# Optimization experiments

Hardware: AMD Instinct MI355X
Metric: run time of the kernel (lower is better)

## Reference

```python
import jax, jax.numpy as jnp
import numpy as np

N_NODES = 100000
N_EDGES = 1600000
F_IN = 256
HID = 256
N_CLS = 16
NUM_PROP = 3


def setup_inputs() -> dict:
    key = jax.random.key(0)
    ks = jax.random.split(key, 8)
    x = jax.random.normal(ks[0], (N_NODES, F_IN), dtype=jnp.float32)
    edge_index = jax.random.randint(ks[1], (2, N_EDGES), 0, N_NODES, dtype=jnp.int64)
    # Glorot-ish scaled weights
    W1 = jax.random.normal(ks[2], (F_IN, HID), dtype=jnp.float32) / np.sqrt(F_IN)
    b1 = jnp.zeros((HID,), dtype=jnp.float32)
    Wi = jax.random.normal(ks[3], (HID, HID), dtype=jnp.float32) / np.sqrt(HID)
    bi = jnp.zeros((HID,), dtype=jnp.float32)
    W2 = jax.random.normal(ks[4], (HID, N_CLS), dtype=jnp.float32) / np.sqrt(HID)
    b2 = jnp.zeros((N_CLS,), dtype=jnp.float32)
    return {"x": x, "edge_index": edge_index, "W1": W1, "b1": b1,
            "Wi": Wi, "bi": bi, "W2": W2, "b2": b2}


def _gcn_graph(edge_index, n_nodes, dtype):
    # PyG GCNConv default: add self-loops, symmetric normalization.
    loop = jnp.arange(n_nodes, dtype=edge_index.dtype)
    src = jnp.concatenate([edge_index[0], loop])  # message source (x_j)
    dst = jnp.concatenate([edge_index[1], loop])  # aggregation target
    deg = jax.ops.segment_sum(jnp.ones_like(dst, dtype=dtype), dst, num_segments=n_nodes)
    dis = jnp.where(deg > 0, jax.lax.rsqrt(jnp.maximum(deg, 1.0)), 0.0)
    norm = dis[src] * dis[dst]  # [E+N]
    return src, dst, norm


def _gcn_conv(h, W, b, src, dst, norm, n_nodes):
    h = h @ W                                   # [N, out]
    msg = h[src] * norm[:, None]                # gather + scale, [E+N, out]
    out = jax.ops.segment_sum(msg, dst, num_segments=n_nodes)
    return out + b


def reference(x, edge_index, W1, b1, Wi, bi, W2, b2):
    n = x.shape[0]
    src, dst, norm = _gcn_graph(edge_index, n, x.dtype)
    h = _gcn_conv(x, W1, b1, src, dst, norm, n)
    # dropout p=0.25 is identity in eval mode (training=False)
    for _ in range(NUM_PROP):
        h = _gcn_conv(h, Wi, bi, src, dst, norm, n)
    h = jax.nn.relu(h)
    h = _gcn_conv(h, W2, b2, src, dst, norm, n)
    return jax.nn.softmax(h, axis=0)  # Softmax(dim=0): over nodes
```

## Files before the change

### kernel.cpp

```cpp
#include <hip/hip_runtime.h>
#include <cstdint>
#include <cstddef>

#define NFEAT 256
#define NCLS  16

typedef unsigned int uint;
typedef unsigned short ushort;
typedef __attribute__((ext_vector_type(8))) short short8;
typedef __attribute__((ext_vector_type(4))) float f32x4;

__device__ inline float blo(uint u) { return __uint_as_float(u << 16); }
__device__ inline float bhi(uint u) { return __uint_as_float(u & 0xffff0000u); }
__device__ inline ushort f2bf(float f) {
    uint b = __float_as_uint(f);
    b += 0x7fffu + ((b >> 16) & 1u);
    return (ushort)(b >> 16);
}
__device__ inline uint pack2(float a, float b) {
    return (uint)f2bf(a) | ((uint)f2bf(b) << 16);
}


__global__ __launch_bounds__(256) void k_ccount(const int* __restrict__ dst,
                                                int* __restrict__ bhist, int E, int nb) {
    __shared__ int h[512];
    int t = threadIdx.x;
    for (int i = t; i < nb; i += 256) h[i] = 0;
    __syncthreads();
    for (int i = blockIdx.x * 256 + t; i < E; i += gridDim.x * 256)
        atomicAdd(&h[dst[i] >> 8], 1);
    __syncthreads();
    for (int i = t; i < nb; i += 256)
        if (h[i]) atomicAdd(&bhist[i], h[i]);
}

__global__ __launch_bounds__(256) void k_cscan(const int* __restrict__ bhist,
                                               int* __restrict__ boff,
                                               int* __restrict__ gcur,
                                               int* __restrict__ rowptr,
                                               int nb, int Nn) {
    int t = threadIdx.x;
    int v0 = (2 * t < nb) ? bhist[2 * t] : 0;
    int v1 = (2 * t + 1 < nb) ? bhist[2 * t + 1] : 0;
    int s = v0 + v1;
    __shared__ int ps[256];
    ps[t] = s;
    __syncthreads();
    for (int off = 1; off < 256; off <<= 1) {
        int v = (t >= off) ? ps[t - off] : 0;
        __syncthreads();
        ps[t] += v;
        __syncthreads();
    }
    int ex = ps[t] - s;
    if (2 * t < nb)     { boff[2 * t] = ex;          gcur[2 * t] = ex; }
    if (2 * t + 1 < nb) { boff[2 * t + 1] = ex + v0; gcur[2 * t + 1] = ex + v0; }
    if (t == 255) { boff[nb] = ps[255]; rowptr[Nn] = ps[255]; }
}

__global__ __launch_bounds__(256) void k_cfill(const int* __restrict__ src,
                                               const int* __restrict__ dst,
                                               int* __restrict__ gcur,
                                               uint2* __restrict__ ebuf, int E, int nb) {
    __shared__ int hist[400];
    __shared__ int lstart[400];
    __shared__ int gbase[400];
    __shared__ int cur[400];
    __shared__ int ps[256];
    __shared__ uint2 stg[4096];
    __shared__ ushort sb[4096];
    int t = threadIdx.x;
    int base = blockIdx.x * 4096;
    int lim = min(4096, E - base);
    for (int i = t; i < nb; i += 256) hist[i] = 0;
    __syncthreads();
    for (int k = t; k < lim; k += 256) atomicAdd(&hist[dst[base + k] >> 8], 1);
    __syncthreads();
    int v0 = (2 * t < nb) ? hist[2 * t] : 0;
    int v1 = (2 * t + 1 < nb) ? hist[2 * t + 1] : 0;
    int s = v0 + v1;
    ps[t] = s;
    __syncthreads();
    for (int off = 1; off < 256; off <<= 1) {
        int v = (t >= off) ? ps[t - off] : 0;
        __syncthreads();
        ps[t] += v;
        __syncthreads();
    }
    int ex = ps[t] - s;
    if (2 * t < nb) {
        lstart[2 * t] = ex; cur[2 * t] = ex;
        if (v0) gbase[2 * t] = atomicAdd(&gcur[2 * t], v0);
    }
    if (2 * t + 1 < nb) {
        lstart[2 * t + 1] = ex + v0; cur[2 * t + 1] = ex + v0;
        if (v1) gbase[2 * t + 1] = atomicAdd(&gcur[2 * t + 1], v1);
    }
    __syncthreads();
    for (int k = t; k < lim; k += 256) {
        int s_ = src[base + k], d_ = dst[base + k];
        int b = d_ >> 8;
        int slot = atomicAdd(&cur[b], 1);
        stg[slot] = make_uint2((uint)s_, (uint)d_);
        sb[slot] = (ushort)b;
    }
    __syncthreads();
    for (int j = t; j < lim; j += 256) {
        int b = sb[j];
        ebuf[gbase[b] + (j - lstart[b])] = stg[j];
    }
}

__global__ __launch_bounds__(256) void k_rowbuild(const uint2* __restrict__ ebuf,
                                                  const int* __restrict__ boff,
                                                  int* __restrict__ rowptr,
                                                  float* __restrict__ dis,
                                                  int* __restrict__ csr_col,
                                                  int Nn, int nb) {
    int b = blockIdx.x;
    int t = threadIdx.x;
    int beg = boff[b], end = boff[b + 1];
    __shared__ int rcnt[256];
    __shared__ int rstart[256];
    __shared__ int ps[256];
    rcnt[t] = 0;
    __syncthreads();
    for (int e = beg + t; e < end; e += 256)
        atomicAdd(&rcnt[ebuf[e].y & 255], 1);
    __syncthreads();
    int v = rcnt[t];
    ps[t] = v;
    __syncthreads();
    for (int off = 1; off < 256; off <<= 1) {
        int u = (t >= off) ? ps[t - off] : 0;
        __syncthreads();
        ps[t] += u;
        __syncthreads();
    }
    int ex = ps[t] - v;
    int node = b * 256 + t;
    if (node < Nn) {
        rowptr[node] = beg + ex;
        dis[node] = rsqrtf((float)(v + 1));
    }
    rstart[t] = beg + ex;
    __syncthreads();
    rcnt[t] = 0;
    __syncthreads();
    for (int e = beg + t; e < end; e += 256) {
        uint2 ed = ebuf[e];
        int r = ed.y & 255;
        int slot = atomicAdd(&rcnt[r], 1);
        csr_col[rstart[r] + slot] = (int)ed.x;
    }
}

__global__ void k_val(const int* __restrict__ col, const float* __restrict__ dis,
                      float* __restrict__ val, int E) {
    int i = blockIdx.x * 256 + threadIdx.x;
    if (i < E) val[i] = dis[col[i]];
}

__global__ __launch_bounds__(256) void k_mm256(const float* __restrict__ A,
                                               const float* __restrict__ B,
                                               float* __restrict__ C) {
    int i = blockIdx.x, j = threadIdx.x;
    float acc = 0.f;
    for (int k = 0; k < 256; ++k) acc = fmaf(A[i * 256 + k], B[k * 256 + j], acc);
    C[i * 256 + j] = acc;
}

__global__ __launch_bounds__(256) void k_vm256(const float* __restrict__ v,
                                               const float* __restrict__ M,
                                               float* __restrict__ r) {
    int j = threadIdx.x;
    float acc = 0.f;
    for (int k = 0; k < 256; ++k) acc = fmaf(v[k], M[(size_t)k * 256 + j], acc);
    r[j] = acc;
}

__global__ __launch_bounds__(256) void k_pack(const float* __restrict__ W,
                                              uint* __restrict__ Wp) {
    int idx = blockIdx.x * 256 + threadIdx.x;
    int w = idx & 3, lane = (idx >> 2) & 63, kstep = (idx >> 8) & 7, n16 = idx >> 11;
    int n = n16 * 16 + (lane & 15);
    int k = kstep * 32 + (lane >> 4) * 8 + 2 * w;
    Wp[idx] = pack2(W[k * 256 + n], W[(k + 1) * 256 + n]);
}

__global__ __launch_bounds__(256) void gemm_mfma(const float* __restrict__ A,
                                                 const uint* __restrict__ Wp,
                                                 ushort* __restrict__ C, int M) {
    int t = threadIdx.x;
    int wv = t >> 6;
    int l = t & 63;
    int m16 = l & 15;
    int kc = l >> 4;
    int bm = blockIdx.x * 64 + wv * 16;
    int bn = blockIdx.y * 64;
    int row = bm + m16;
    bool valid = row < M;
    const float* ap = A + (size_t)(valid ? row : 0) * 256 + kc * 8;
    const short8* wp = (const short8*)Wp;
    int n16b = bn >> 4;

    f32x4 acc0 = {0.f, 0.f, 0.f, 0.f};
    f32x4 acc1 = acc0, acc2 = acc0, acc3 = acc0;

#pragma unroll
    for (int ks = 0; ks < 8; ++ks) {
        float4 fa0 = make_float4(0.f, 0.f, 0.f, 0.f), fa1 = fa0;
        if (valid) {
            fa0 = *(const float4*)(ap + ks * 32);
            fa1 = *(const float4*)(ap + ks * 32 + 4);
        }
        short8 a;
        a[0] = (short)f2bf(fa0.x); a[1] = (short)f2bf(fa0.y);
        a[2] = (short)f2bf(fa0.z); a[3] = (short)f2bf(fa0.w);
        a[4] = (short)f2bf(fa1.x); a[5] = (short)f2bf(fa1.y);
        a[6] = (short)f2bf(fa1.z); a[7] = (short)f2bf(fa1.w);
        short8 b0 = wp[((n16b + 0) * 8 + ks) * 64 + l];
        short8 b1 = wp[((n16b + 1) * 8 + ks) * 64 + l];
        short8 b2 = wp[((n16b + 2) * 8 + ks) * 64 + l];
        short8 b3 = wp[((n16b + 3) * 8 + ks) * 64 + l];
        acc0 = __builtin_amdgcn_mfma_f32_16x16x32_bf16(a, b0, acc0, 0, 0, 0);
        acc1 = __builtin_amdgcn_mfma_f32_16x16x32_bf16(a, b1, acc1, 0, 0, 0);
        acc2 = __builtin_amdgcn_mfma_f32_16x16x32_bf16(a, b2, acc2, 0, 0, 0);
        acc3 = __builtin_amdgcn_mfma_f32_16x16x32_bf16(a, b3, acc3, 0, 0, 0);
    }

#pragma unroll
    for (int r = 0; r < 4; ++r) {
        int orow = bm + kc * 4 + r;
        if (orow < M) {
            ushort* cp = C + (size_t)orow * 256 + bn + m16;
            cp[0]  = f2bf(acc0[r]);
            cp[16] = f2bf(acc1[r]);
            cp[32] = f2bf(acc2[r]);
            cp[48] = f2bf(acc3[r]);
        }
    }
}

template <int FIRST>
__global__ __launch_bounds__(256) void k_svec(const float* __restrict__ sin,
                                              const int* __restrict__ rowptr,
                                              const int* __restrict__ col,
                                              const float* __restrict__ val,
                                              const float* __restrict__ dis,
                                              float* __restrict__ sout, int Nn) {
    int d = blockIdx.x * 256 + threadIdx.x;
    if (d >= Nn) return;
    int beg = rowptr[d], end = rowptr[d + 1];
    float acc = 0.f;
    if (FIRST) {
        for (int e = beg; e < end; ++e) acc += val[e];
    } else {
        for (int e = beg; e < end; ++e) acc = fmaf(val[e], sin[col[e]], acc);
    }
    float dd = dis[d];
    sout[d] = fmaf(dd, acc, dd * dd * (FIRST ? 1.f : sin[d]));
}

template <int FINAL>
__global__ __launch_bounds__(64) void k_aggb(const uint* __restrict__ y,
                                             const int* __restrict__ rowptr,
                                             const int* __restrict__ col,
                                             const float* __restrict__ val,
                                             const float* __restrict__ dis,
                                             const float* __restrict__ s1,
                                             const float* __restrict__ s2,
                                             const float* __restrict__ s3,
                                             const float* __restrict__ c1,
                                             const float* __restrict__ c2,
                                             const float* __restrict__ c3,
                                             const float* __restrict__ c4,
                                             uint* __restrict__ out) {
    int d = blockIdx.x;
    int t = threadIdx.x;
    const uint* yt = y + 2 * t;
    int beg = rowptr[d], end = rowptr[d + 1];
    float a0 = 0.f, a1 = 0.f, a2 = 0.f, a3 = 0.f;
    int e = beg;
    for (; e + 3 < end; e += 4) {
        int   cA = col[e],     cB = col[e + 1], cC = col[e + 2], cD = col[e + 3];
        float vA = val[e],     vB = val[e + 1], vC = val[e + 2], vD = val[e + 3];
        uint2 uA = *(const uint2*)(yt + (size_t)cA * 128);
        uint2 uB = *(const uint2*)(yt + (size_t)cB * 128);
        uint2 uC = *(const uint2*)(yt + (size_t)cC * 128);
        uint2 uD = *(const uint2*)(yt + (size_t)cD * 128);
        a0 = fmaf(vA, blo(uA.x), a0); a1 = fmaf(vA, bhi(uA.x), a1);
        a2 = fmaf(vA, blo(uA.y), a2); a3 = fmaf(vA, bhi(uA.y), a3);
        a0 = fmaf(vB, blo(uB.x), a0); a1 = fmaf(vB, bhi(uB.x), a1);
        a2 = fmaf(vB, blo(uB.y), a2); a3 = fmaf(vB, bhi(uB.y), a3);
        a0 = fmaf(vC, blo(uC.x), a0); a1 = fmaf(vC, bhi(uC.x), a1);
        a2 = fmaf(vC, blo(uC.y), a2); a3 = fmaf(vC, bhi(uC.y), a3);
        a0 = fmaf(vD, blo(uD.x), a0); a1 = fmaf(vD, bhi(uD.x), a1);
        a2 = fmaf(vD, blo(uD.y), a2); a3 = fmaf(vD, bhi(uD.y), a3);
    }
    for (; e < end; ++e) {
        int c = col[e]; float v = val[e];
        uint2 u = *(const uint2*)(yt + (size_t)c * 128);
        a0 = fmaf(v, blo(u.x), a0); a1 = fmaf(v, bhi(u.x), a1);
        a2 = fmaf(v, blo(u.y), a2); a3 = fmaf(v, bhi(u.y), a3);
    }
    float dd = dis[d];
    float d2 = dd * dd;
    uint2 us = *(const uint2*)(yt + (size_t)d * 128);
    float r0 = fmaf(dd, a0, d2 * blo(us.x));
    float r1 = fmaf(dd, a1, d2 * bhi(us.x));
    float r2 = fmaf(dd, a2, d2 * blo(us.y));
    float r3 = fmaf(dd, a3, d2 * bhi(us.y));
    if (FINAL) {
        float4 C1 = *(const float4*)(c1 + 4 * t);
        float4 C2 = *(const float4*)(c2 + 4 * t);
        float4 C3 = *(const float4*)(c3 + 4 * t);
        float4 C4 = *(const float4*)(c4 + 4 * t);
        float S1 = s1[d], S2 = s2[d], S3 = s3[d];
        r0 += S3 * C1.x + S2 * C2.x + S1 * C3.x + C4.x;
        r1 += S3 * C1.y + S2 * C2.y + S1 * C3.y + C4.y;
        r2 += S3 * C1.z + S2 * C2.z + S1 * C3.z + C4.z;
        r3 += S3 * C1.w + S2 * C2.w + S1 * C3.w + C4.w;
    }
    uint2 o;
    o.x = pack2(r0, r1);
    o.y = pack2(r2, r3);
    *(uint2*)(out + (size_t)d * 128 + 2 * t) = o;
}

__global__ __launch_bounds__(256) void k_gemm16b(const uint* __restrict__ A,
                                                 const float* __restrict__ W2,
                                                 float* __restrict__ Y, int M) {
    __shared__ float Ws[256][16];
    int t = threadIdx.x;
    for (int i = t; i < 256 * 16; i += 256) Ws[i >> 4][i & 15] = W2[i];
    __syncthreads();
    int tx = t & 15, ty = t >> 4;
    int r = blockIdx.x * 16 + ty;
    if (r >= M) return;
    const uint* a = A + (size_t)r * 128;
    float acc = 0.f;
    for (int i = 0; i < 128; i += 4) {
        uint4 u = *(const uint4*)(a + i);
        float f;
        f = fmaxf(blo(u.x), 0.f); acc = fmaf(f, Ws[2 * i + 0][tx], acc);
        f = fmaxf(bhi(u.x), 0.f); acc = fmaf(f, Ws[2 * i + 1][tx], acc);
        f = fmaxf(blo(u.y), 0.f); acc = fmaf(f, Ws[2 * i + 2][tx], acc);
        f = fmaxf(bhi(u.y), 0.f); acc = fmaf(f, Ws[2 * i + 3][tx], acc);
        f = fmaxf(blo(u.z), 0.f); acc = fmaf(f, Ws[2 * i + 4][tx], acc);
        f = fmaxf(bhi(u.z), 0.f); acc = fmaf(f, Ws[2 * i + 5][tx], acc);
        f = fmaxf(blo(u.w), 0.f); acc = fmaf(f, Ws[2 * i + 6][tx], acc);
        f = fmaxf(bhi(u.w), 0.f); acc = fmaf(f, Ws[2 * i + 7][tx], acc);
    }
    Y[(size_t)r * NCLS + tx] = acc;
}

__global__ __launch_bounds__(256) void k_agg16(const float* __restrict__ y16,
                                               const int* __restrict__ rowptr,
                                               const int* __restrict__ col,
                                               const float* __restrict__ val,
                                               const float* __restrict__ dis,
                                               const float* __restrict__ b2,
                                               float* __restrict__ out, int Nn) {
    int t = threadIdx.x;
    int tx = t & 15, ty = t >> 4;
    int d = blockIdx.x * 16 + ty;
    if (d >= Nn) return;
    int beg = rowptr[d], end = rowptr[d + 1];
    float acc = 0.f;
    for (int e = beg; e < end; ++e)
        acc = fmaf(val[e], y16[(size_t)col[e] * NCLS + tx], acc);
    float dd = dis[d];
    out[(size_t)d * NCLS + tx] = dd * acc + dd * dd * y16[(size_t)d * NCLS + tx] + b2[tx];
}

__global__ __launch_bounds__(256) void k_sm1(const float* __restrict__ z,
                                             float* __restrict__ pmax,
                                             float* __restrict__ psum, int Nn) {
    int b = blockIdx.x, t = threadIdx.x, tx = t & 15, ty = t >> 4;
    int CH = (Nn + 255) / 256;
    int r0 = b * CH, r1 = min(r0 + CH, Nn);
    __shared__ float red[16][17];
    __shared__ float gloc[16];
    float m = -3.4e38f;
    for (int r = r0 + ty; r < r1; r += 16) m = fmaxf(m, z[(size_t)r * NCLS + tx]);
    red[ty][tx] = m;
    __syncthreads();
    if (ty == 0) {
        float mm = red[0][tx];
#pragma unroll
        for (int i = 1; i < 16; ++i) mm = fmaxf(mm, red[i][tx]);
        gloc[tx] = mm;
    }
    __syncthreads();
    float g = gloc[tx];
    float s = 0.f;
    for (int r = r0 + ty; r < r1; r += 16) s += expf(z[(size_t)r * NCLS + tx] - g);
    red[ty][tx] = s;
    __syncthreads();
    if (ty == 0) {
        float ss = red[0][tx];
#pragma unroll
        for (int i = 1; i < 16; ++i) ss += red[i][tx];
        pmax[b * 16 + tx] = g;
        psum[b * 16 + tx] = ss;
    }
}

__global__ __launch_bounds__(256) void k_sm2(const float* __restrict__ pmax,
                                             const float* __restrict__ psum,
                                             float* __restrict__ g16,
                                             float* __restrict__ inv16) {
    int t = threadIdx.x, tx = t & 15, ty = t >> 4;
    __shared__ float red[16][17];
    __shared__ float gsh[16];
    float m = -3.4e38f;
    for (int b = ty; b < 256; b += 16) m = fmaxf(m, pmax[b * 16 + tx]);
    red[ty][tx] = m;
    __syncthreads();
    if (ty == 0) {
        float mm = red[0][tx];
#pragma unroll
        for (int i = 1; i < 16; ++i) mm = fmaxf(mm, red[i][tx]);
        gsh[tx] = mm;
    }
    __syncthreads();
    float g = gsh[tx];
    float s = 0.f;
    for (int b = ty; b < 256; b += 16)
        s += psum[b * 16 + tx] * expf(pmax[b * 16 + tx] - g);
    red[ty][tx] = s;
    __syncthreads();
    if (ty == 0) {
        float ss = red[0][tx];
#pragma unroll
        for (int i = 1; i < 16; ++i) ss += red[i][tx];
        g16[tx] = g;
        inv16[tx] = 1.0f / ss;
    }
}

__global__ void k_sm5(float* __restrict__ z, const float* __restrict__ g16,
                      const float* __restrict__ inv16, int total) {
    int i = blockIdx.x * 256 + threadIdx.x;
    if (i < total) {
        int c = i & 15;
        z[i] = expf(z[i] - g16[c]) * inv16[c];
    }
}

extern "C" void kernel_launch(void* const* d_in, const int* in_sizes, int n_in,
                              void* d_out, int out_size, void* d_ws, size_t ws_size,
                              hipStream_t stream) {
    const float* x  = (const float*)d_in[0];
    const int*   ei = (const int*)d_in[1];
    const float* W1 = (const float*)d_in[2];
    const float* b1 = (const float*)d_in[3];
    const float* Wi = (const float*)d_in[4];
    const float* bi = (const float*)d_in[5];
    const float* W2 = (const float*)d_in[6];
    const float* b2 = (const float*)d_in[7];
    float* out = (float*)d_out;

    int Nn = in_sizes[0] / NFEAT;
    int E  = in_sizes[1] / 2;
    int nb = (Nn + 255) >> 8;
    const int* esrc = ei;
    const int* edst = ei + E;

    char* p = (char*)d_ws;
    auto carve = [&](size_t bytes) -> char* {
        char* r = p;
        p += (bytes + 255) / 256 * 256;
        return r;
    };
    uint*  bufA    = (uint*) carve((size_t)Nn * 128 * 4);
    uint*  bufB    = (uint*) carve((size_t)Nn * 128 * 4);
    int*   rowptr  = (int*)  carve((size_t)(Nn + 1) * 4);
    float* dis     = (float*)carve((size_t)Nn * 4);
    int*   csr_col = (int*)  carve((size_t)E * 4);
    float* csr_val = (float*)carve((size_t)E * 4);
    uint2* ebuf    = (uint2*)carve((size_t)E * 8);
    int*   bhist   = (int*)  carve(512 * 4);
    int*   boff    = (int*)  carve(512 * 4);
    int*   gcur    = (int*)  carve(512 * 4);
    float* y16     = (float*)carve((size_t)Nn * NCLS * 4);
    float* s1      = (float*)carve((size_t)Nn * 4);
    float* s2      = (float*)carve((size_t)Nn * 4);
    float* s3      = (float*)carve((size_t)Nn * 4);
    float* WA      = (float*)carve(256 * 256 * 4);
    float* WB      = (float*)carve(256 * 256 * 4);
    float* Wc      = (float*)carve(256 * 256 * 4);
    uint*  Wp      = (uint*) carve(32768 * 4);
    float* c1      = (float*)carve(256 * 4);
    float* c2      = (float*)carve(256 * 4);
    float* c3      = (float*)carve(256 * 4);
    float* u1      = (float*)carve(256 * 4);
    float* u2      = (float*)carve(256 * 4);
    float* pmax    = (float*)carve(256 * 16 * 4);
    float* psum    = (float*)carve(256 * 16 * 4);
    float* g16     = (float*)carve(16 * 4);
    float* inv16   = (float*)carve(16 * 4);

    hipMemsetAsync(bhist, 0, 512 * 4, stream);

    int gE = (E + 255) / 256;
    int gN = (Nn + 255) / 256;
    int nch = (E + 4095) / 4096;

    k_ccount<<<1024, 256, 0, stream>>>(edst, bhist, E, nb);
    k_cscan<<<1, 256, 0, stream>>>(bhist, boff, gcur, rowptr, nb, Nn);
    k_cfill<<<nch, 256, 0, stream>>>(esrc, edst, gcur, ebuf, E, nb);
    k_rowbuild<<<nb, 256, 0, stream>>>(ebuf, boff, rowptr, dis, csr_col, Nn, nb);
    k_val<<<gE, 256, 0, stream>>>(csr_col, dis, csr_val, E);

    k_mm256<<<256, 256, 0, stream>>>(W1, Wi, WA);
    k_mm256<<<256, 256, 0, stream>>>(WA, Wi, WB);
    k_mm256<<<256, 256, 0, stream>>>(WB, Wi, Wc);
    k_pack<<<128, 256, 0, stream>>>(Wc, Wp);
    k_vm256<<<1, 256, 0, stream>>>(bi, Wi, c3);
    k_vm256<<<1, 256, 0, stream>>>(c3, Wi, c2);
    k_vm256<<<1, 256, 0, stream>>>(b1, Wi, u1);
    k_vm256<<<1, 256, 0, stream>>>(u1, Wi, u2);
    k_vm256<<<1, 256, 0, stream>>>(u2, Wi, c1);

    k_svec<1><<<gN, 256, 0, stream>>>(nullptr, rowptr, csr_col, csr_val, dis, s1, Nn);
    k_svec<0><<<gN, 256, 0, stream>>>(s1, rowptr, csr_col, csr_val, dis, s2, Nn);
    k_svec<0><<<gN, 256, 0, stream>>>(s2, rowptr, csr_col, csr_val, dis, s3, Nn);

    dim3 gg((Nn + 63) / 64, 4);
    gemm_mfma<<<gg, 256, 0, stream>>>(x, Wp, (ushort*)bufB, Nn);

    k_aggb<0><<<Nn, 64, 0, stream>>>(bufB, rowptr, csr_col, csr_val, dis,
                                     nullptr, nullptr, nullptr, nullptr, nullptr, nullptr, nullptr, bufA);
    k_aggb<0><<<Nn, 64, 0, stream>>>(bufA, rowptr, csr_col, csr_val, dis,
                                     nullptr, nullptr, nullptr, nullptr, nullptr, nullptr, nullptr, bufB);
    k_aggb<0><<<Nn, 64, 0, stream>>>(bufB, rowptr, csr_col, csr_val, dis,
                                     nullptr, nullptr, nullptr, nullptr, nullptr, nullptr, nullptr, bufA);
    k_aggb<1><<<Nn, 64, 0, stream>>>(bufA, rowptr, csr_col, csr_val, dis,
                                     s1, s2, s3, c1, c2, c3, bi, bufB);

    int g16b = (Nn + 15) / 16;
    k_gemm16b<<<g16b, 256, 0, stream>>>(bufB, W2, y16, Nn);
    k_agg16<<<g16b, 256, 0, stream>>>(y16, rowptr, csr_col, csr_val, dis, b2, out, Nn);

    k_sm1<<<256, 256, 0, stream>>>(out, pmax, psum, Nn);
    k_sm2<<<1, 256, 0, stream>>>(pmax, psum, g16, inv16);
    k_sm5<<<(Nn * NCLS + 255) / 256, 256, 0, stream>>>(out, g16, inv16, Nn * NCLS);
}
```

Measured before the change: 902.5 us.

## Widen GEMM to full 256 columns per block and pack four nodes per aggregation block

```diff
diff --git a/kernel.cpp b/kernel.cpp
--- a/kernel.cpp
+++ b/kernel.cpp
@@ -20,7 +20,6 @@
 __device__ inline uint pack2(float a, float b) {
     return (uint)f2bf(a) | ((uint)f2bf(b) << 16);
 }
-
 
 __global__ __launch_bounds__(256) void k_ccount(const int* __restrict__ dst,
                                                 int* __restrict__ bhist, int E, int nb) {
@@ -198,17 +197,15 @@
     int m16 = l & 15;
     int kc = l >> 4;
     int bm = blockIdx.x * 64 + wv * 16;
-    int bn = blockIdx.y * 64;
     int row = bm + m16;
     bool valid = row < M;
     const float* ap = A + (size_t)(valid ? row : 0) * 256 + kc * 8;
     const short8* wp = (const short8*)Wp;
-    int n16b = bn >> 4;
-
-    f32x4 acc0 = {0.f, 0.f, 0.f, 0.f};
-    f32x4 acc1 = acc0, acc2 = acc0, acc3 = acc0;
-
-#pragma unroll
+
+    f32x4 acc[16];
+#pragma unroll
+    for (int n = 0; n < 16; ++n) acc[n] = {0.f, 0.f, 0.f, 0.f};
+
     for (int ks = 0; ks < 8; ++ks) {
         float4 fa0 = make_float4(0.f, 0.f, 0.f, 0.f), fa1 = fa0;
         if (valid) {
@@ -220,25 +217,20 @@
         a[2] = (short)f2bf(fa0.z); a[3] = (short)f2bf(fa0.w);
         a[4] = (short)f2bf(fa1.x); a[5] = (short)f2bf(fa1.y);
         a[6] = (short)f2bf(fa1.z); a[7] = (short)f2bf(fa1.w);
-        short8 b0 = wp[((n16b + 0) * 8 + ks) * 64 + l];
-        short8 b1 = wp[((n16b + 1) * 8 + ks) * 64 + l];
-        short8 b2 = wp[((n16b + 2) * 8 + ks) * 64 + l];
-        short8 b3 = wp[((n16b + 3) * 8 + ks) * 64 + l];
-        acc0 = __builtin_amdgcn_mfma_f32_16x16x32_bf16(a, b0, acc0, 0, 0, 0);
-        acc1 = __builtin_amdgcn_mfma_f32_16x16x32_bf16(a, b1, acc1, 0, 0, 0);
-        acc2 = __builtin_amdgcn_mfma_f32_16x16x32_bf16(a, b2, acc2, 0, 0, 0);
-        acc3 = __builtin_amdgcn_mfma_f32_16x16x32_bf16(a, b3, acc3, 0, 0, 0);
+#pragma unroll
+        for (int n = 0; n < 16; ++n) {
+            short8 b = wp[(n * 8 + ks) * 64 + l];
+            acc[n] = __builtin_amdgcn_mfma_f32_16x16x32_bf16(a, b, acc[n], 0, 0, 0);
+        }
     }
 
 #pragma unroll
     for (int r = 0; r < 4; ++r) {
         int orow = bm + kc * 4 + r;
         if (orow < M) {
-            ushort* cp = C + (size_t)orow * 256 + bn + m16;
-            cp[0]  = f2bf(acc0[r]);
-            cp[16] = f2bf(acc1[r]);
-            cp[32] = f2bf(acc2[r]);
-            cp[48] = f2bf(acc3[r]);
+            ushort* cp = C + (size_t)orow * 256 + m16;
+#pragma unroll
+            for (int n = 0; n < 16; ++n) cp[n * 16] = f2bf(acc[n][r]);
         }
     }
 }
@@ -264,40 +256,55 @@
 }
 
 template <int FINAL>
-__global__ __launch_bounds__(64) void k_aggb(const uint* __restrict__ y,
-                                             const int* __restrict__ rowptr,
-                                             const int* __restrict__ col,
-                                             const float* __restrict__ val,
-                                             const float* __restrict__ dis,
-                                             const float* __restrict__ s1,
-                                             const float* __restrict__ s2,
-                                             const float* __restrict__ s3,
-                                             const float* __restrict__ c1,
-                                             const float* __restrict__ c2,
-                                             const float* __restrict__ c3,
-                                             const float* __restrict__ c4,
-                                             uint* __restrict__ out) {
-    int d = blockIdx.x;
-    int t = threadIdx.x;
+__global__ __launch_bounds__(256) void k_aggb(const uint* __restrict__ y,
+                                              const int* __restrict__ rowptr,
+                                              const int* __restrict__ col,
+                                              const float* __restrict__ val,
+                                              const float* __restrict__ dis,
+                                              const float* __restrict__ s1,
+                                              const float* __restrict__ s2,
+                                              const float* __restrict__ s3,
+                                              const float* __restrict__ c1,
+                                              const float* __restrict__ c2,
+                                              const float* __restrict__ c3,
+                                              const float* __restrict__ c4,
+                                              uint* __restrict__ out, int Nn) {
+    int wid = threadIdx.x >> 6;
+    int t = threadIdx.x & 63;
+    int d = blockIdx.x * 4 + wid;
+    if (d >= Nn) return;
     const uint* yt = y + 2 * t;
     int beg = rowptr[d], end = rowptr[d + 1];
     float a0 = 0.f, a1 = 0.f, a2 = 0.f, a3 = 0.f;
     int e = beg;
-    for (; e + 3 < end; e += 4) {
-        int   cA = col[e],     cB = col[e + 1], cC = col[e + 2], cD = col[e + 3];
-        float vA = val[e],     vB = val[e + 1], vC = val[e + 2], vD = val[e + 3];
-        uint2 uA = *(const uint2*)(yt + (size_t)cA * 128);
-        uint2 uB = *(const uint2*)(yt + (size_t)cB * 128);
-        uint2 uC = *(const uint2*)(yt + (size_t)cC * 128);
-        uint2 uD = *(const uint2*)(yt + (size_t)cD * 128);
-        a0 = fmaf(vA, blo(uA.x), a0); a1 = fmaf(vA, bhi(uA.x), a1);
-        a2 = fmaf(vA, blo(uA.y), a2); a3 = fmaf(vA, bhi(uA.y), a3);
-        a0 = fmaf(vB, blo(uB.x), a0); a1 = fmaf(vB, bhi(uB.x), a1);
-        a2 = fmaf(vB, blo(uB.y), a2); a3 = fmaf(vB, bhi(uB.y), a3);
-        a0 = fmaf(vC, blo(uC.x), a0); a1 = fmaf(vC, bhi(uC.x), a1);
-        a2 = fmaf(vC, blo(uC.y), a2); a3 = fmaf(vC, bhi(uC.y), a3);
-        a0 = fmaf(vD, blo(uD.x), a0); a1 = fmaf(vD, bhi(uD.x), a1);
-        a2 = fmaf(vD, blo(uD.y), a2); a3 = fmaf(vD, bhi(uD.y), a3);
+    for (; e + 7 < end; e += 8) {
+        int cc[8]; float vv[8]; uint2 uu[8];
+#pragma unroll
+        for (int j = 0; j < 8; ++j) { cc[j] = col[e + j]; vv[j] = val[e + j]; }
+#pragma unroll
+        for (int j = 0; j < 8; ++j) uu[j] = *(const uint2*)(yt + (size_t)cc[j] * 128);
+#pragma unroll
+        for (int j = 0; j < 8; ++j) {
+            a0 = fmaf(vv[j], blo(uu[j].x), a0);
+            a1 = fmaf(vv[j], bhi(uu[j].x), a1);
+            a2 = fmaf(vv[j], blo(uu[j].y), a2);
+            a3 = fmaf(vv[j], bhi(uu[j].y), a3);
+        }
+    }
+    if (e + 3 < end) {
+        int cc[4]; float vv[4]; uint2 uu[4];
+#pragma unroll
+        for (int j = 0; j < 4; ++j) { cc[j] = col[e + j]; vv[j] = val[e + j]; }
+#pragma unroll
+        for (int j = 0; j < 4; ++j) uu[j] = *(const uint2*)(yt + (size_t)cc[j] * 128);
+#pragma unroll
+        for (int j = 0; j < 4; ++j) {
+            a0 = fmaf(vv[j], blo(uu[j].x), a0);
+            a1 = fmaf(vv[j], bhi(uu[j].x), a1);
+            a2 = fmaf(vv[j], blo(uu[j].y), a2);
+            a3 = fmaf(vv[j], bhi(uu[j].y), a3);
+        }
+        e += 4;
     }
     for (; e < end; ++e) {
         int c = col[e]; float v = val[e];
@@ -529,17 +536,17 @@
     k_svec<0><<<gN, 256, 0, stream>>>(s1, rowptr, csr_col, csr_val, dis, s2, Nn);
     k_svec<0><<<gN, 256, 0, stream>>>(s2, rowptr, csr_col, csr_val, dis, s3, Nn);
 
-    dim3 gg((Nn + 63) / 64, 4);
-    gemm_mfma<<<gg, 256, 0, stream>>>(x, Wp, (ushort*)bufB, Nn);
-
-    k_aggb<0><<<Nn, 64, 0, stream>>>(bufB, rowptr, csr_col, csr_val, dis,
-                                     nullptr, nullptr, nullptr, nullptr, nullptr, nullptr, nullptr, bufA);
-    k_aggb<0><<<Nn, 64, 0, stream>>>(bufA, rowptr, csr_col, csr_val, dis,
-                                     nullptr, nullptr, nullptr, nullptr, nullptr, nullptr, nullptr, bufB);
-    k_aggb<0><<<Nn, 64, 0, stream>>>(bufB, rowptr, csr_col, csr_val, dis,
-                                     nullptr, nullptr, nullptr, nullptr, nullptr, nullptr, nullptr, bufA);
-    k_aggb<1><<<Nn, 64, 0, stream>>>(bufA, rowptr, csr_col, csr_val, dis,
-                                     s1, s2, s3, c1, c2, c3, bi, bufB);
+    gemm_mfma<<<(Nn + 63) / 64, 256, 0, stream>>>(x, Wp, (ushort*)bufB, Nn);
+
+    int gA = (Nn + 3) / 4;
+    k_aggb<0><<<gA, 256, 0, stream>>>(bufB, rowptr, csr_col, csr_val, dis,
+                                      nullptr, nullptr, nullptr, nullptr, nullptr, nullptr, nullptr, bufA, Nn);
+    k_aggb<0><<<gA, 256, 0, stream>>>(bufA, rowptr, csr_col, csr_val, dis,
+                                      nullptr, nullptr, nullptr, nullptr, nullptr, nullptr, nullptr, bufB, Nn);
+    k_aggb<0><<<gA, 256, 0, stream>>>(bufB, rowptr, csr_col, csr_val, dis,
+                                      nullptr, nullptr, nullptr, nullptr, nullptr, nullptr, nullptr, bufA, Nn);
+    k_aggb<1><<<gA, 256, 0, stream>>>(bufA, rowptr, csr_col, csr_val, dis,
+                                      s1, s2, s3, c1, c2, c3, bi, bufB, Nn);
 
     int g16b = (Nn + 15) / 16;
     k_gemm16b<<<g16b, 256, 0, stream>>>(bufB, W2, y16, Nn);
```

Result: no change. 918.7 us (+1.8%).
